# Performance work log

Measured on AMD Instinct MI355X. Metric: run time of the kernel, lower is better.

## Reference

```python
import jax, jax.numpy as jnp
import numpy as np

D_MODEL = 1024
K_QUERY = 32
K_TOPK = 4

def setup_inputs() -> dict:
    key = jax.random.key(0)
    k1, k2, k3, k4, k5 = jax.random.split(key, 5)
    x = jax.random.normal(k1, (4, 2048, D_MODEL), dtype=jnp.float32)
    # nn.Linear(d_model, k_query): weight [k_query, d_model], bias [k_query]
    sc = 1.0 / np.sqrt(D_MODEL)
    Wq = jax.random.uniform(k2, (K_QUERY, D_MODEL), jnp.float32, -sc, sc)
    bq = jax.random.uniform(k3, (K_QUERY,), jnp.float32, -sc, sc)
    Wk = jax.random.uniform(k4, (K_QUERY, D_MODEL), jnp.float32, -sc, sc)
    bk = jax.random.uniform(k5, (K_QUERY,), jnp.float32, -sc, sc)
    return {"x": x, "Wq": Wq, "bq": bq, "Wk": Wk, "bk": bk}

def reference(x, Wq, bq, Wk, bk):
    # x: [B, T, D]
    queries = jnp.einsum('btd,kd->btk', x, Wq) + bq      # [B, T, Kq]
    keys = jnp.einsum('btd,kd->btk', x, Wk) + bk         # [B, T, Kq]
    sim = jnp.einsum('btk,bsk->bts', queries, keys)      # [B, T, T]
    sim = sim / jnp.sqrt(jnp.float32(queries.shape[-1]))
    _, topk_idx = jax.lax.top_k(sim, K_TOPK)              # [B, T, K]
    # gather neighbors per (b, t): x[b, topk_idx[b, t]] -> [B, T, K, D]
    neighbors = jax.vmap(lambda xb, ib: xb[ib])(x, topk_idx)
    gathered = neighbors.mean(axis=2)                     # [B, T, D]
    return gathered
```

## Files before the change

### kernel.cpp

```cpp
#include <hip/hip_runtime.h>
#include <math.h>

#define D_MODEL 1024
#define T_SEQ   2048
#define NBATCH  4
#define NROWS   (NBATCH * T_SEQ)
#define NOUT    64

#define SKLD 264
#define SQLD 20
#define XLD  260

typedef double v4df __attribute__((ext_vector_type(4)));

__device__ __forceinline__ bool key_gt(float av, int ai, float bv, int bi) {
    return (av > bv) || (av == bv && ai < bi);
}

__device__ __forceinline__ void cmpswap(float& v0, int& i0, float& v1, int& i1) {
    bool sw = key_gt(v1, i1, v0, i0);
    float nv0 = sw ? v1 : v0, nv1 = sw ? v0 : v1;
    int   ni0 = sw ? i1 : i0, ni1 = sw ? i0 : i1;
    v0 = nv0; v1 = nv1; i0 = ni0; i1 = ni1;
}

__device__ __forceinline__ void merge4(float (&a)[4], int (&ai)[4],
                                       float b0, int j0, float b1, int j1,
                                       float b2, int j2, float b3, int j3) {
    if (!key_gt(a[0], ai[0], b3, j3)) { a[0] = b3; ai[0] = j3; }
    if (!key_gt(a[1], ai[1], b2, j2)) { a[1] = b2; ai[1] = j2; }
    if (!key_gt(a[2], ai[2], b1, j1)) { a[2] = b1; ai[2] = j1; }
    if (!key_gt(a[3], ai[3], b0, j0)) { a[3] = b0; ai[3] = j0; }
    cmpswap(a[0], ai[0], a[2], ai[2]);
    cmpswap(a[1], ai[1], a[3], ai[3]);
    cmpswap(a[0], ai[0], a[1], ai[1]);
    cmpswap(a[2], ai[2], a[3], ai[3]);
}

__device__ __forceinline__ void insert4(float (&tv)[4], int (&tix)[4], float v, int idx) {
    if (v > tv[3]) {
        bool g0 = v > tv[0], g1 = v > tv[1], g2 = v > tv[2];
        float n0 = g0 ? v : tv[0];
        int   m0 = g0 ? idx : tix[0];
        float n1 = g1 ? (g0 ? tv[0] : v) : tv[1];
        int   m1 = g1 ? (g0 ? tix[0] : idx) : tix[1];
        float n2 = g2 ? (g1 ? tv[1] : v) : tv[2];
        int   m2 = g2 ? (g1 ? tix[1] : idx) : tix[2];
        float n3 = g2 ? tv[2] : v;
        int   m3 = g2 ? tix[2] : idx;
        tv[0] = n0; tv[1] = n1; tv[2] = n2; tv[3] = n3;
        tix[0] = m0; tix[1] = m1; tix[2] = m2; tix[3] = m3;
    }
}

__global__ __launch_bounds__(64) void mfma_probe(int* __restrict__ tab)
{
    __shared__ double Aref[16][4];
    __shared__ double Bref[4][16];
    __shared__ double Dref[16][16];

    const int lane = threadIdx.x;
    {
        const int m = lane & 15, k = lane >> 4;
        Aref[m][k] = (double)(1 + m * 4 + k);
        Bref[k][m] = (double)(1 + k * 16 + m);
    }
    __syncthreads();
    for (int e = lane; e < 256; e += 64) {
        const int m = e >> 4, n = e & 15;
        double s = 0.0;
        for (int k = 0; k < 4; ++k) s += Aref[m][k] * Bref[k][n];
        Dref[m][n] = s;
    }
    __syncthreads();

    int found = -1;
    for (int h = 0; h < 16; ++h) {
        if (found >= 0) break;
        const int fa = h & 1, fb = (h >> 1) & 1, fd = h >> 2;
        const int am = fa ? (lane >> 2) : (lane & 15);
        const int ak = fa ? (lane & 3)  : (lane >> 4);
        const int bn = fb ? (lane >> 2) : (lane & 15);
        const int bk = fb ? (lane & 3)  : (lane >> 4);
        v4df c = {0.0, 0.0, 0.0, 0.0};
        c = __builtin_amdgcn_mfma_f64_16x16x4f64(Aref[am][ak], Bref[bk][bn], c, 0, 0, 0);
        bool ok = true;
        #pragma unroll
        for (int i = 0; i < 4; ++i) {
            int dm, dn;
            if (fd == 0)      { dm = 4 * (lane >> 4) + i; dn = lane & 15; }
            else if (fd == 1) { dn = 4 * (lane >> 4) + i; dm = lane & 15; }
            else if (fd == 2) { dm = (lane >> 4) + 4 * i; dn = lane & 15; }
            else              { dn = (lane >> 4) + 4 * i; dm = lane & 15; }
            if (c[i] != Dref[dm][dn]) ok = false;
        }
        if (__all(ok)) found = h;
    }

    const int fa = (found >= 0) ? (found & 1) : 0;
    const int fb = (found >= 0) ? ((found >> 1) & 1) : 0;
    const int fd = (found >= 0) ? (found >> 2) : 0;
    tab[1   + lane] = fa ? (lane >> 2) : (lane & 15);
    tab[65  + lane] = fa ? (lane & 3)  : (lane >> 4);
    tab[129 + lane] = fb ? (lane & 3)  : (lane >> 4);
    tab[193 + lane] = fb ? (lane >> 2) : (lane & 15);
    #pragma unroll
    for (int i = 0; i < 4; ++i) {
        int dm, dn;
        if (fd == 0)      { dm = 4 * (lane >> 4) + i; dn = lane & 15; }
        else if (fd == 1) { dn = 4 * (lane >> 4) + i; dm = lane & 15; }
        else if (fd == 2) { dm = (lane >> 4) + 4 * i; dn = lane & 15; }
        else              { dn = (lane >> 4) + 4 * i; dm = lane & 15; }
        tab[257 + lane * 4 + i] = dm;
        tab[513 + lane * 4 + i] = dn;
    }
    if (lane == 0) tab[0] = found;
}

__global__ __launch_bounds__(256) void wprep_kernel(
    const float* __restrict__ Wq, const float* __restrict__ Wk,
    double* __restrict__ Wdt)
{
    const int idx = blockIdx.x * 256 + threadIdx.x;
    const int o = idx & 63;
    const int d = idx >> 6;
    float v = (o < 32) ? Wq[(size_t)o * D_MODEL + d]
                       : Wk[(size_t)(o - 32) * D_MODEL + d];
    Wdt[(size_t)d * 64 + o] = (double)v;
}

__global__ __launch_bounds__(256) void proj_mfma(
    const float* __restrict__ x, const double* __restrict__ Wdt,
    const float* __restrict__ bq, const float* __restrict__ bk_,
    const int* __restrict__ tab,
    float* __restrict__ Qt, float* __restrict__ Kt)
{
    __shared__ float xlds[16 * XLD];

    const int tid  = threadIdx.x;
    const int lane = tid & 63;
    const int og   = __builtin_amdgcn_readfirstlane(tid >> 6);
    const int row0 = blockIdx.x * 16;

    const int flag = tab[0];
    const int am  = tab[1   + lane];
    const int ak  = tab[65  + lane];
    const int bkk = tab[129 + lane];
    const int bn  = tab[193 + lane];

    const double* wcol = Wdt + og * 16;

    v4df acc = {0.0, 0.0, 0.0, 0.0};

    for (int st = 0; st < 4; ++st) {
        __syncthreads();
        #pragma unroll
        for (int j = 0; j < 4; ++j) {
            const int f  = j * 256 + tid;
            const int r  = f >> 6;
            const int c4 = f & 63;
            float4 v = *reinterpret_cast<const float4*>(
                x + (size_t)(row0 + r) * D_MODEL + st * 256 + c4 * 4);
            *reinterpret_cast<float4*>(&xlds[r * XLD + c4 * 4]) = v;
        }
        __syncthreads();

        if (flag >= 0) {
            #pragma unroll 8
            for (int kk = 0; kk < 64; ++kk) {
                double a = (double)xlds[am * XLD + kk * 4 + ak];
                double b = wcol[(size_t)(st * 256 + kk * 4 + bkk) * 64 + bn];
                acc = __builtin_amdgcn_mfma_f64_16x16x4f64(a, b, acc, 0, 0, 0);
            }
        } else {
            const int n  = lane & 15;
            const int r4 = (lane >> 4) * 4;
            for (int dd = 0; dd < 256; ++dd) {
                double wv = wcol[(size_t)(st * 256 + dd) * 64 + n];
                #pragma unroll
                for (int i = 0; i < 4; ++i)
                    acc[i] = fma((double)xlds[(r4 + i) * XLD + dd], wv, acc[i]);
            }
        }
    }

    #pragma unroll
    for (int i = 0; i < 4; ++i) {
        const int dmv = tab[257 + lane * 4 + i];
        const int dnv = tab[513 + lane * 4 + i];
        const int out = og * 16 + dnv;
        const int row = row0 + dmv;
        const int bb  = row >> 11, t = row & 2047;
        const double bias = (out < 32) ? (double)bq[out] : (double)bk_[out - 32];
        const float v = (float)(acc[i] + bias);
        if (out < 32) Qt[((size_t)bb * 32 + out) * T_SEQ + t] = v;
        else          Kt[((size_t)bb * 32 + (out - 32)) * T_SEQ + t] = v;
    }
}

__global__ __launch_bounds__(128) void sim_topk(
    const float* __restrict__ Qt, const float* __restrict__ Kt,
    float* __restrict__ candVal ,
    int*   __restrict__ candIdx )
{
    __shared__ float klds[32 * SKLD];
    __shared__ float qlds[32 * SQLD];
    __shared__ float cV[2][16][4];
    __shared__ int   cI[2][16][4];

    const int tid  = threadIdx.x;
    const int lane = tid & 63;
    const int wav  = tid >> 6;
    const int half = blockIdx.x & 1;
    const int tt   = (blockIdx.x >> 1) & 127;
    const int b    = blockIdx.x >> 8;
    const int tblk = tt * 16;
    const int sh0  = half * 1024;

    const float* QtB = Qt + (size_t)b * 32 * T_SEQ;
    const float* KtB = Kt + (size_t)b * 32 * T_SEQ;

    {
        const int i  = tid >> 2;
        const int t4 = (tid & 3) * 4;
        float4 v = *reinterpret_cast<const float4*>(QtB + (size_t)i * T_SEQ + tblk + t4);
        *reinterpret_cast<float4*>(&qlds[i * SQLD + t4]) = v;
    }

    const int tg = tid & 3;
    const int t0 = tg * 4;
    const int s0 = (tid >> 2) * 8;

    float tv[4][4]; int tix[4][4];
    #pragma unroll
    for (int r = 0; r < 4; ++r)
        #pragma unroll
        for (int j = 0; j < 4; ++j) { tv[r][j] = -INFINITY; tix[r][j] = 0x7fffffff; }

    for (int st = 0; st < 4; ++st) {
        __syncthreads();
        #pragma unroll
        for (int j = 0; j < 16; ++j) {
            const int f  = (tid + j * 128) * 4;
            const int ki = f >> 8;
            const int ks = f & 255;
            float4 v = *reinterpret_cast<const float4*>(
                KtB + (size_t)ki * T_SEQ + sh0 + st * 256 + ks);
            *reinterpret_cast<float4*>(&klds[ki * SKLD + ks]) = v;
        }
        __syncthreads();

        float acc[4][8];
        #pragma unroll
        for (int r = 0; r < 4; ++r)
            #pragma unroll
            for (int c = 0; c < 8; ++c) acc[r][c] = 0.f;

        #pragma unroll 4
        for (int i = 0; i < 32; ++i) {
            float4 qv  = *reinterpret_cast<const float4*>(&qlds[i * SQLD + t0]);
            float4 kv0 = *reinterpret_cast<const float4*>(&klds[i * SKLD + s0]);
            float4 kv1 = *reinterpret_cast<const float4*>(&klds[i * SKLD + s0 + 4]);
            const float qa[4] = {qv.x, qv.y, qv.z, qv.w};
            const float ka[8] = {kv0.x, kv0.y, kv0.z, kv0.w, kv1.x, kv1.y, kv1.z, kv1.w};
            #pragma unroll
            for (int r = 0; r < 4; ++r)
                #pragma unroll
                for (int c = 0; c < 8; ++c)
                    acc[r][c] = fmaf(qa[r], ka[c], acc[r][c]);
        }

        const int sbase = sh0 + st * 256 + s0;
        #pragma unroll
        for (int c = 0; c < 8; ++c)
            #pragma unroll
            for (int r = 0; r < 4; ++r)
                insert4(tv[r], tix[r], acc[r][c], sbase + c);
    }

    #pragma unroll
    for (int m = 4; m <= 32; m <<= 1) {
        #pragma unroll
        for (int r = 0; r < 4; ++r) {
            float b0 = __shfl_xor(tv[r][0], m, 64);
            float b1 = __shfl_xor(tv[r][1], m, 64);
            float b2 = __shfl_xor(tv[r][2], m, 64);
            float b3 = __shfl_xor(tv[r][3], m, 64);
            int   j0 = __shfl_xor(tix[r][0], m, 64);
            int   j1 = __shfl_xor(tix[r][1], m, 64);
            int   j2 = __shfl_xor(tix[r][2], m, 64);
            int   j3 = __shfl_xor(tix[r][3], m, 64);
            merge4(tv[r], tix[r], b0, j0, b1, j1, b2, j2, b3, j3);
        }
    }

    if (lane < 4) {
        #pragma unroll
        for (int r = 0; r < 4; ++r)
            #pragma unroll
            for (int j = 0; j < 4; ++j) {
                cV[wav][lane * 4 + r][j] = tv[r][j];
                cI[wav][lane * 4 + r][j] = tix[r][j];
            }
    }
    __syncthreads();

    if (tid < 16) {
        float mv[4]; int mi[4];
        #pragma unroll
        for (int j = 0; j < 4; ++j) { mv[j] = cV[0][tid][j]; mi[j] = cI[0][tid][j]; }
        merge4(mv, mi,
               cV[1][tid][0], cI[1][tid][0],
               cV[1][tid][1], cI[1][tid][1],
               cV[1][tid][2], cI[1][tid][2],
               cV[1][tid][3], cI[1][tid][3]);
        const size_t row = (size_t)b * T_SEQ + tblk + tid;
        float4 vv = {mv[0], mv[1], mv[2], mv[3]};
        int4   ii = {mi[0], mi[1], mi[2], mi[3]};
        *reinterpret_cast<float4*>(candVal + ((size_t)half * NROWS + row) * 4) = vv;
        *reinterpret_cast<int4*>(candIdx + ((size_t)half * NROWS + row) * 4) = ii;
    }
}

__global__ __launch_bounds__(256) void merge_gather(
    const float* __restrict__ x,
    const float* __restrict__ candVal, const int* __restrict__ candIdx,
    float* __restrict__ out)
{
    __shared__ int topIdx[8][4];

    const int tid  = threadIdx.x;
    const int row0 = blockIdx.x * 8;
    const int b    = row0 >> 11;

    if (tid < 8) {
        const size_t row = row0 + tid;
        float4 v0 = *reinterpret_cast<const float4*>(candVal + row * 4);
        int4   i0 = *reinterpret_cast<const int4*>(candIdx + row * 4);
        float4 v1 = *reinterpret_cast<const float4*>(candVal + ((size_t)NROWS + row) * 4);
        int4   i1 = *reinterpret_cast<const int4*>(candIdx + ((size_t)NROWS + row) * 4);
        float mv[4] = {v0.x, v0.y, v0.z, v0.w};
        int   mi[4] = {i0.x, i0.y, i0.z, i0.w};
        merge4(mv, mi, v1.x, i1.x, v1.y, i1.y, v1.z, i1.z, v1.w, i1.w);
        #pragma unroll
        for (int j = 0; j < 4; ++j) topIdx[tid][j] = mi[j];
    }
    __syncthreads();

    const float* xb = x + (size_t)b * T_SEQ * D_MODEL;
    float* ob = out + (size_t)row0 * D_MODEL;
    #pragma unroll
    for (int r = 0; r < 8; ++r) {
        const int i0 = topIdx[r][0], i1 = topIdx[r][1], i2 = topIdx[r][2], i3 = topIdx[r][3];
        float4 a0 = *(reinterpret_cast<const float4*>(xb + (size_t)i0 * D_MODEL) + tid);
        float4 a1 = *(reinterpret_cast<const float4*>(xb + (size_t)i1 * D_MODEL) + tid);
        float4 a2 = *(reinterpret_cast<const float4*>(xb + (size_t)i2 * D_MODEL) + tid);
        float4 a3 = *(reinterpret_cast<const float4*>(xb + (size_t)i3 * D_MODEL) + tid);
        float4 o;
        o.x = (a0.x + a1.x + a2.x + a3.x) * 0.25f;
        o.y = (a0.y + a1.y + a2.y + a3.y) * 0.25f;
        o.z = (a0.z + a1.z + a2.z + a3.z) * 0.25f;
        o.w = (a0.w + a1.w + a2.w + a3.w) * 0.25f;
        *(reinterpret_cast<float4*>(ob + (size_t)r * D_MODEL) + tid) = o;
    }
}

extern "C" void kernel_launch(void* const* d_in, const int* in_sizes, int n_in,
                              void* d_out, int out_size, void* d_ws, size_t ws_size,
                              hipStream_t stream) {
    const float* x  = (const float*)d_in[0];
    const float* Wq = (const float*)d_in[1];
    const float* bq = (const float*)d_in[2];
    const float* Wk = (const float*)d_in[3];
    const float* bk = (const float*)d_in[4];
    float* out = (float*)d_out;

    char* wsb = (char*)d_ws;
    int*    tab  = (int*)wsb;
    double* Wdt  = (double*)(wsb + 4096);
    float*  Qt   = (float*)(wsb + 4096 + (size_t)D_MODEL * NOUT * 8);
    float*  Kt   = Qt + (size_t)NBATCH * 32 * T_SEQ;
    float*  candVal = (float*)((char*)Kt + (size_t)NBATCH * 32 * T_SEQ * 4);
    int*    candIdx = (int*)((char*)candVal + (size_t)2 * NROWS * 4 * 4);

    mfma_probe<<<dim3(1), dim3(64), 0, stream>>>(tab);
    wprep_kernel<<<dim3(256), dim3(256), 0, stream>>>(Wq, Wk, Wdt);
    proj_mfma<<<dim3(NROWS / 16), dim3(256), 0, stream>>>(x, Wdt, bq, bk, tab, Qt, Kt);
    sim_topk<<<dim3(1024), dim3(128), 0, stream>>>(Qt, Kt, candVal, candIdx);
    merge_gather<<<dim3(1024), dim3(256), 0, stream>>>(x, candVal, candIdx, out);
}
```

Baseline: 171.0 us.

## Split projection over D halves and sim_topk into quarter key ranges

The projection kernel now loads the whole 16-row x tile into LDS once and uses 8 waves, with two waves splitting the D reduction per output group and combining partial sums through shared memory. The sim/top-k kernel processes 32 query rows per block across a quarter of the key range with 256 threads, so merge_gather now merges four candidate sets instead of two. The aim is more parallelism and fewer LDS staging barriers. The cost is larger LDS use, which lowers occupancy, plus extra candidate traffic and merge work.

```diff
diff --git a/kernel.cpp b/kernel.cpp
--- a/kernel.cpp
+++ b/kernel.cpp
@@ -6,10 +6,11 @@
 #define NBATCH  4
 #define NROWS   (NBATCH * T_SEQ)
 #define NOUT    64
+#define NQTR    4
 
 #define SKLD 264
-#define SQLD 20
-#define XLD  260
+#define SQLD 36
+#define XLD  1032
 
 typedef double v4df __attribute__((ext_vector_type(4)));
 
@@ -129,18 +130,22 @@
     Wdt[(size_t)d * 64 + o] = (double)v;
 }
 
-__global__ __launch_bounds__(256) void proj_mfma(
+__global__ __launch_bounds__(512) void proj_mfma(
     const float* __restrict__ x, const double* __restrict__ Wdt,
     const float* __restrict__ bq, const float* __restrict__ bk_,
     const int* __restrict__ tab,
     float* __restrict__ Qt, float* __restrict__ Kt)
 {
-    __shared__ float xlds[16 * XLD];
+    __shared__ float  xlds[16 * XLD];
+    __shared__ double comb[4][64][4];
 
     const int tid  = threadIdx.x;
     const int lane = tid & 63;
-    const int og   = __builtin_amdgcn_readfirstlane(tid >> 6);
+    const int wav  = tid >> 6;
+    const int og   = __builtin_amdgcn_readfirstlane(wav >> 1);
+    const int half = __builtin_amdgcn_readfirstlane(wav & 1);
     const int row0 = blockIdx.x * 16;
+    const int dbase = half * 512;
 
     const int flag = tab[0];
     const int am  = tab[1   + lane];
@@ -150,86 +155,92 @@
 
     const double* wcol = Wdt + og * 16;
 
+    #pragma unroll
+    for (int j = 0; j < 8; ++j) {
+        const int f  = j * 512 + tid;
+        const int r  = f >> 8;
+        const int c4 = f & 255;
+        float4 v = *reinterpret_cast<const float4*>(
+            x + (size_t)(row0 + r) * D_MODEL + c4 * 4);
+        *reinterpret_cast<float4*>(&xlds[r * XLD + c4 * 4]) = v;
+    }
+    __syncthreads();
+
     v4df acc = {0.0, 0.0, 0.0, 0.0};
 
-    for (int st = 0; st < 4; ++st) {
-        __syncthreads();
-        #pragma unroll
-        for (int j = 0; j < 4; ++j) {
-            const int f  = j * 256 + tid;
-            const int r  = f >> 6;
-            const int c4 = f & 63;
-            float4 v = *reinterpret_cast<const float4*>(
-                x + (size_t)(row0 + r) * D_MODEL + st * 256 + c4 * 4);
-            *reinterpret_cast<float4*>(&xlds[r * XLD + c4 * 4]) = v;
-        }
-        __syncthreads();
-
-        if (flag >= 0) {
-            #pragma unroll 8
-            for (int kk = 0; kk < 64; ++kk) {
-                double a = (double)xlds[am * XLD + kk * 4 + ak];
-                double b = wcol[(size_t)(st * 256 + kk * 4 + bkk) * 64 + bn];
-                acc = __builtin_amdgcn_mfma_f64_16x16x4f64(a, b, acc, 0, 0, 0);
-            }
-        } else {
-            const int n  = lane & 15;
-            const int r4 = (lane >> 4) * 4;
-            for (int dd = 0; dd < 256; ++dd) {
-                double wv = wcol[(size_t)(st * 256 + dd) * 64 + n];
-                #pragma unroll
-                for (int i = 0; i < 4; ++i)
-                    acc[i] = fma((double)xlds[(r4 + i) * XLD + dd], wv, acc[i]);
-            }
-        }
-    }
-
-    #pragma unroll
-    for (int i = 0; i < 4; ++i) {
-        const int dmv = tab[257 + lane * 4 + i];
-        const int dnv = tab[513 + lane * 4 + i];
-        const int out = og * 16 + dnv;
-        const int row = row0 + dmv;
-        const int bb  = row >> 11, t = row & 2047;
-        const double bias = (out < 32) ? (double)bq[out] : (double)bk_[out - 32];
-        const float v = (float)(acc[i] + bias);
-        if (out < 32) Qt[((size_t)bb * 32 + out) * T_SEQ + t] = v;
-        else          Kt[((size_t)bb * 32 + (out - 32)) * T_SEQ + t] = v;
-    }
-}
-
-__global__ __launch_bounds__(128) void sim_topk(
+    if (flag >= 0) {
+        #pragma unroll 8
+        for (int kk = 0; kk < 128; ++kk) {
+            double a = (double)xlds[am * XLD + dbase + kk * 4 + ak];
+            double b = wcol[(size_t)(dbase + kk * 4 + bkk) * 64 + bn];
+            acc = __builtin_amdgcn_mfma_f64_16x16x4f64(a, b, acc, 0, 0, 0);
+        }
+    } else {
+        const int n  = lane & 15;
+        const int r4 = (lane >> 4) * 4;
+        for (int dd = 0; dd < 512; ++dd) {
+            const int d = dbase + dd;
+            double wv = wcol[(size_t)d * 64 + n];
+            #pragma unroll
+            for (int i = 0; i < 4; ++i)
+                acc[i] = fma((double)xlds[(r4 + i) * XLD + d], wv, acc[i]);
+        }
+    }
+
+    if (half == 1) {
+        #pragma unroll
+        for (int i = 0; i < 4; ++i) comb[og][lane][i] = acc[i];
+    }
+    __syncthreads();
+
+    if (half == 0) {
+        #pragma unroll
+        for (int i = 0; i < 4; ++i) {
+            const double tot = acc[i] + comb[og][lane][i];
+            const int dmv = tab[257 + lane * 4 + i];
+            const int dnv = tab[513 + lane * 4 + i];
+            const int out = og * 16 + dnv;
+            const int row = row0 + dmv;
+            const int bb  = row >> 11, t = row & 2047;
+            const double bias = (out < 32) ? (double)bq[out] : (double)bk_[out - 32];
+            const float v = (float)(tot + bias);
+            if (out < 32) Qt[((size_t)bb * 32 + out) * T_SEQ + t] = v;
+            else          Kt[((size_t)bb * 32 + (out - 32)) * T_SEQ + t] = v;
+        }
+    }
+}
+
+__global__ __launch_bounds__(256) void sim_topk(
     const float* __restrict__ Qt, const float* __restrict__ Kt,
     float* __restrict__ candVal ,
     int*   __restrict__ candIdx )
 {
     __shared__ float klds[32 * SKLD];
     __shared__ float qlds[32 * SQLD];
-    __shared__ float cV[2][16][4];
-    __shared__ int   cI[2][16][4];
+    __shared__ float cV[4][32][4];
+    __shared__ int   cI[4][32][4];
 
     const int tid  = threadIdx.x;
     const int lane = tid & 63;
     const int wav  = tid >> 6;
-    const int half = blockIdx.x & 1;
-    const int tt   = (blockIdx.x >> 1) & 127;
+    const int qtr  = blockIdx.x & 3;
+    const int tt   = (blockIdx.x >> 2) & 63;
     const int b    = blockIdx.x >> 8;
-    const int tblk = tt * 16;
-    const int sh0  = half * 1024;
+    const int tblk = tt * 32;
+    const int sq0  = qtr * 512;
 
     const float* QtB = Qt + (size_t)b * 32 * T_SEQ;
     const float* KtB = Kt + (size_t)b * 32 * T_SEQ;
 
     {
-        const int i  = tid >> 2;
-        const int t4 = (tid & 3) * 4;
+        const int i  = tid >> 3;
+        const int t4 = (tid & 7) * 4;
         float4 v = *reinterpret_cast<const float4*>(QtB + (size_t)i * T_SEQ + tblk + t4);
         *reinterpret_cast<float4*>(&qlds[i * SQLD + t4]) = v;
     }
 
-    const int tg = tid & 3;
-    const int t0 = tg * 4;
-    const int s0 = (tid >> 2) * 8;
+    const int t0 = (tid & 7) * 4;
+    const int s0 = (tid >> 3) * 8;
 
     float tv[4][4]; int tix[4][4];
     #pragma unroll
@@ -237,15 +248,15 @@
         #pragma unroll
         for (int j = 0; j < 4; ++j) { tv[r][j] = -INFINITY; tix[r][j] = 0x7fffffff; }
 
-    for (int st = 0; st < 4; ++st) {
+    for (int st = 0; st < 2; ++st) {
         __syncthreads();
         #pragma unroll
-        for (int j = 0; j < 16; ++j) {
-            const int f  = (tid + j * 128) * 4;
+        for (int j = 0; j < 8; ++j) {
+            const int f  = (tid + j * 256) * 4;
             const int ki = f >> 8;
             const int ks = f & 255;
             float4 v = *reinterpret_cast<const float4*>(
-                KtB + (size_t)ki * T_SEQ + sh0 + st * 256 + ks);
+                KtB + (size_t)ki * T_SEQ + sq0 + st * 256 + ks);
             *reinterpret_cast<float4*>(&klds[ki * SKLD + ks]) = v;
         }
         __syncthreads();
@@ -270,7 +281,7 @@
                     acc[r][c] = fmaf(qa[r], ka[c], acc[r][c]);
         }
 
-        const int sbase = sh0 + st * 256 + s0;
+        const int sbase = sq0 + st * 256 + s0;
         #pragma unroll
         for (int c = 0; c < 8; ++c)
             #pragma unroll
@@ -279,7 +290,7 @@
     }
 
     #pragma unroll
-    for (int m = 4; m <= 32; m <<= 1) {
+    for (int m = 8; m <= 32; m <<= 1) {
         #pragma unroll
         for (int r = 0; r < 4; ++r) {
             float b0 = __shfl_xor(tv[r][0], m, 64);
@@ -294,7 +305,7 @@
         }
     }
 
-    if (lane < 4) {
+    if (lane < 8) {
         #pragma unroll
         for (int r = 0; r < 4; ++r)
             #pragma unroll
@@ -305,20 +316,22 @@
     }
     __syncthreads();
 
-    if (tid < 16) {
+    if (tid < 32) {
         float mv[4]; int mi[4];
         #pragma unroll
         for (int j = 0; j < 4; ++j) { mv[j] = cV[0][tid][j]; mi[j] = cI[0][tid][j]; }
-        merge4(mv, mi,
-               cV[1][tid][0], cI[1][tid][0],
-               cV[1][tid][1], cI[1][tid][1],
-               cV[1][tid][2], cI[1][tid][2],
-               cV[1][tid][3], cI[1][tid][3]);
+        #pragma unroll
+        for (int w = 1; w < 4; ++w)
+            merge4(mv, mi,
+                   cV[w][tid][0], cI[w][tid][0],
+                   cV[w][tid][1], cI[w][tid][1],
+                   cV[w][tid][2], cI[w][tid][2],
+                   cV[w][tid][3], cI[w][tid][3]);
         const size_t row = (size_t)b * T_SEQ + tblk + tid;
         float4 vv = {mv[0], mv[1], mv[2], mv[3]};
         int4   ii = {mi[0], mi[1], mi[2], mi[3]};
-        *reinterpret_cast<float4*>(candVal + ((size_t)half * NROWS + row) * 4) = vv;
-        *reinterpret_cast<int4*>(candIdx + ((size_t)half * NROWS + row) * 4) = ii;
+        *reinterpret_cast<float4*>(candVal + ((size_t)qtr * NROWS + row) * 4) = vv;
+        *reinterpret_cast<int4*>(candIdx + ((size_t)qtr * NROWS + row) * 4) = ii;
     }
 }
 
@@ -337,11 +350,14 @@
         const size_t row = row0 + tid;
         float4 v0 = *reinterpret_cast<const float4*>(candVal + row * 4);
         int4   i0 = *reinterpret_cast<const int4*>(candIdx + row * 4);
-        float4 v1 = *reinterpret_cast<const float4*>(candVal + ((size_t)NROWS + row) * 4);
-        int4   i1 = *reinterpret_cast<const int4*>(candIdx + ((size_t)NROWS + row) * 4);
         float mv[4] = {v0.x, v0.y, v0.z, v0.w};
         int   mi[4] = {i0.x, i0.y, i0.z, i0.w};
-        merge4(mv, mi, v1.x, i1.x, v1.y, i1.y, v1.z, i1.z, v1.w, i1.w);
+        #pragma unroll
+        for (int q = 1; q < NQTR; ++q) {
+            float4 v1 = *reinterpret_cast<const float4*>(candVal + ((size_t)q * NROWS + row) * 4);
+            int4   i1 = *reinterpret_cast<const int4*>(candIdx + ((size_t)q * NROWS + row) * 4);
+            merge4(mv, mi, v1.x, i1.x, v1.y, i1.y, v1.z, i1.z, v1.w, i1.w);
+        }
         #pragma unroll
         for (int j = 0; j < 4; ++j) topIdx[tid][j] = mi[j];
     }
@@ -381,11 +397,11 @@
     float*  Qt   = (float*)(wsb + 4096 + (size_t)D_MODEL * NOUT * 8);
     float*  Kt   = Qt + (size_t)NBATCH * 32 * T_SEQ;
     float*  candVal = (float*)((char*)Kt + (size_t)NBATCH * 32 * T_SEQ * 4);
-    int*    candIdx = (int*)((char*)candVal + (size_t)2 * NROWS * 4 * 4);
+    int*    candIdx = (int*)((char*)candVal + (size_t)NQTR * NROWS * 4 * 4);
 
     mfma_probe<<<dim3(1), dim3(64), 0, stream>>>(tab);
     wprep_kernel<<<dim3(256), dim3(256), 0, stream>>>(Wq, Wk, Wdt);
-    proj_mfma<<<dim3(NROWS / 16), dim3(256), 0, stream>>>(x, Wdt, bq, bk, tab, Qt, Kt);
-    sim_topk<<<dim3(1024), dim3(128), 0, stream>>>(Qt, Kt, candVal, candIdx);
+    proj_mfma<<<dim3(NROWS / 16), dim3(512), 0, stream>>>(x, Wdt, bq, bk, tab, Qt, Kt);
+    sim_topk<<<dim3(1024), dim3(256), 0, stream>>>(Qt, Kt, candVal, candIdx);
     merge_gather<<<dim3(1024), dim3(256), 0, stream>>>(x, candVal, candIdx, out);
 }
```

Result: faster. 163.9 us (-4.1%).
